# Kernel optimization log

Measured on AMD Instinct MI355X. Metric: run time of the kernel, lower is better.

Reference implementation:

```python
import jax, jax.numpy as jnp
import numpy as np
from jax import lax

B, N, T, H, V, C = 256, 196, 26, 512, 12000, 1000


def setup_inputs() -> dict:
    key = jax.random.key(0)
    ks = jax.random.split(key, 24)
    g = lambda i, shape, s=0.02: jax.random.normal(ks[i], shape, jnp.float32) * s
    z = lambda *shape: jnp.zeros(shape, jnp.float32)
    return {
        "image": jax.random.normal(ks[0], (B, N, H), jnp.float32),
        "question": jax.random.randint(ks[1], (B, T), 0, V, jnp.int32),
        "embed_table": g(2, (V, H), 1.0),
        "W_img": g(3, (H, H)), "b_img": z(H),
        "W_uni": g(4, (1, H, H)), "b_uni": z(H),
        "W_bi": g(5, (2, H, H)), "b_bi": z(H),
        "W_tri": g(6, (3, H, H)), "b_tri": z(H),
        "lstm_k": g(7, (H, 4 * H)), "lstm_rk": g(8, (H, 4 * H)), "lstm_b": z(4 * H),
        "W_corr": g(9, (H, H)), "b_corr": z(H),
        "W_qe": g(10, (H, H)), "b_qe": z(H),
        "W_ie": g(11, (H, H)), "b_ie": z(H),
        "w_qa": g(12, (H, 1)), "b_qa": z(1),
        "w_ia": g(13, (H, 1)), "b_ia": z(1),
        "W_w": g(14, (H, H)), "b_w": z(H),
        "W_p": g(15, (2 * H, H)), "b_p": z(H),
        "W_s": g(16, (2 * H, H)), "b_s": z(H),
        "W_fc1": g(17, (H, 2 * H)), "b_fc1": z(2 * H),
        "W_fc": g(18, (2 * H, C)), "b_fc": z(C),
    }


def _conv1d(x, w, b, dil):
    # x: [B,T,H], w: [k, in, out] (WIO). TF 'same' padding == XLA SAME.
    y = lax.conv_general_dilated(x, w, window_strides=(1,), padding='SAME',
                                 rhs_dilation=(dil,),
                                 dimension_numbers=('NWC', 'WIO', 'NWC'))
    return y + b


def _lstm(x, k, rk, b):
    # Keras LSTM, gate order i,f,c,o; inference (dropout off).
    xp = jnp.einsum('bth,hg->btg', x, k) + b  # [B,T,4H]
    h0 = jnp.zeros((x.shape[0], rk.shape[0]), x.dtype)

    def step(carry, xt):
        h, c = carry
        zg = xt + h @ rk
        i, f, g, o = jnp.split(zg, 4, axis=-1)
        i, f, o = jax.nn.sigmoid(i), jax.nn.sigmoid(f), jax.nn.sigmoid(o)
        c = f * c + i * jnp.tanh(g)
        h = o * jnp.tanh(c)
        return (h, c), h

    _, hs = lax.scan(step, (h0, h0), jnp.swapaxes(xp, 0, 1))
    return jnp.swapaxes(hs, 0, 1)  # [B,T,H]


def _co_attention(img_feat, ques_feat, W_corr, b_corr, W_qe, b_qe, W_ie, b_ie,
                  w_qa, b_qa, w_ia, b_ia):
    img_corr = img_feat @ W_corr + b_corr                       # [B,N,H]
    wm = jnp.tanh(jnp.einsum('btd,bnd->btn', ques_feat, img_corr))  # affinity
    ques_embed = ques_feat @ W_qe + b_qe                        # [B,T,H]
    img_embed = img_feat @ W_ie + b_ie                          # [B,N,H]
    ques_sum = jnp.tanh(jnp.einsum('btn,bnd->btd', wm, img_embed) + ques_embed)
    ques_att = jax.nn.softmax((ques_sum @ w_qa + b_qa)[..., 0], axis=-1)  # [B,T]
    img_sum = jnp.tanh(jnp.einsum('btn,btd->bnd', wm, ques_embed) + img_embed)
    img_att = jax.nn.softmax((img_sum @ w_ia + b_ia)[..., 0], axis=-1)    # [B,N]
    q_feat = jnp.einsum('bt,btd->bd', ques_att, ques_feat)
    v_feat = jnp.einsum('bn,bnd->bd', img_att, img_feat)
    return v_feat, q_feat


def reference(image, question, embed_table, W_img, b_img, W_uni, b_uni, W_bi, b_bi,
              W_tri, b_tri, lstm_k, lstm_rk, lstm_b, W_corr, b_corr, W_qe, b_qe,
              W_ie, b_ie, w_qa, b_qa, w_ia, b_ia, W_w, b_w, W_p, b_p, W_s, b_s,
              W_fc1, b_fc1, W_fc, b_fc):
    img = jnp.tanh(image @ W_img + b_img)                       # [B,N,H]
    words = embed_table[question]                               # [B,T,H]
    uni = jnp.tanh(_conv1d(words, W_uni, b_uni, 1))
    bi = jnp.tanh(_conv1d(words, W_bi, b_bi, 2))
    tri = jnp.tanh(_conv1d(words, W_tri, b_tri, 2))
    phrase = jnp.tanh(jnp.maximum(jnp.maximum(uni, bi), tri))   # maxpool over 3 n-grams
    sentence = _lstm(phrase, lstm_k, lstm_rk, lstm_b)
    ca = lambda v, q: _co_attention(v, q, W_corr, b_corr, W_qe, b_qe, W_ie, b_ie,
                                    w_qa, b_qa, w_ia, b_ia)
    v_word, q_word = ca(img, words)
    v_phr, q_phr = ca(img, phrase)
    v_sent, q_sent = ca(img, sentence)
    h_w = jnp.tanh((q_word + v_word) @ W_w + b_w)
    h_p = jnp.tanh(jnp.concatenate([q_phr + v_phr, h_w], axis=1) @ W_p + b_p)
    h_s = jnp.tanh(jnp.concatenate([q_sent + v_sent, h_p], axis=1) @ W_s + b_s)
    fc1 = jax.nn.relu(h_s @ W_fc1 + b_fc1)
    return jax.nn.softmax(fc1 @ W_fc + b_fc, axis=-1)           # [B,C]
```

## Files before the change

### kernel.cpp

```cpp
#include <hip/hip_runtime.h>
#include <hip/hip_bf16.h>
#include <math.h>

#define Bq   256
#define Nimg 196
#define Tseq 26
#define Hd   512
#define H4   2048
#define Ccls 1000
#define KP   1536

typedef int   int4v  __attribute__((ext_vector_type(4)));
typedef float f32x4  __attribute__((ext_vector_type(4)));

#define SWZ8(x) ((x) ^ (((x) >> 3) & 7))

__device__ __forceinline__ float fast_tanh(float x) {
    float e = __expf(2.0f * x);
    return 1.0f - 2.0f * __builtin_amdgcn_rcpf(e + 1.0f);
}
__device__ __forceinline__ float fast_sigmoid(float x) {
    return __builtin_amdgcn_rcpf(1.0f + __expf(-x));
}

__device__ __forceinline__ short f2bf(float x) {
    union { float f; unsigned u; } a; a.f = x;
    unsigned r = a.u + 0x7FFF + ((a.u >> 16) & 1);
    return (short)(r >> 16);
}
__device__ __forceinline__ float bf2f(short b) {
    union { float f; unsigned u; } a; a.u = ((unsigned)(unsigned short)b) << 16;
    return a.f;
}

__global__ void embed_kernel(const int* __restrict__ q, const float* __restrict__ table,
                             short* __restrict__ words2) {
    int row = blockIdx.x;
    int tok = q[row];
    int c4 = threadIdx.x * 4;
    float4 v = *reinterpret_cast<const float4*>(table + (size_t)tok * Hd + c4);
    short h0 = f2bf(v.x), h1 = f2bf(v.y), h2 = f2bf(v.z), h3 = f2bf(v.w);
    short l0 = f2bf(v.x - bf2f(h0)), l1 = f2bf(v.y - bf2f(h1));
    short l2 = f2bf(v.z - bf2f(h2)), l3 = f2bf(v.w - bf2f(h3));
    *reinterpret_cast<short4*>(words2 + (size_t)row * 1024 + c4) = make_short4(h0, h1, h2, h3);
    *reinterpret_cast<short4*>(words2 + (size_t)row * 1024 + 512 + c4) = make_short4(l0, l1, l2, l3);
}

__global__ void split_kernel(const float* __restrict__ X, short* __restrict__ X2) {
    int i4 = blockIdx.x * 256 + threadIdx.x;
    int m = i4 >> 7, c4 = (i4 & 127) * 4;
    float4 v = *reinterpret_cast<const float4*>(X + ((size_t)m << 9) + c4);
    short h0 = f2bf(v.x), h1 = f2bf(v.y), h2 = f2bf(v.z), h3 = f2bf(v.w);
    short l0 = f2bf(v.x - bf2f(h0)), l1 = f2bf(v.y - bf2f(h1));
    short l2 = f2bf(v.z - bf2f(h2)), l3 = f2bf(v.w - bf2f(h3));
    *reinterpret_cast<short4*>(X2 + (size_t)m * 1024 + c4) = make_short4(h0, h1, h2, h3);
    *reinterpret_cast<short4*>(X2 + (size_t)m * 1024 + 512 + c4) = make_short4(l0, l1, l2, l3);
}

__global__ __launch_bounds__(256) void wsplit_kernel(const float* __restrict__ W, int Nw,
                                                     short* __restrict__ WT2) {
    __shared__ float tile[64][65];
    const int n0 = blockIdx.x * 64, k0 = blockIdx.y * 64;
    const int tid = threadIdx.x;
    #pragma unroll
    for (int p = 0; p < 16; ++p) {
        int r = p * 4 + (tid >> 6);
        int c = tid & 63;
        tile[r][c] = W[(size_t)(k0 + r) * Nw + n0 + c];
    }
    __syncthreads();
    const int n = tid >> 2;
    const int ksub = (tid & 3) * 16;
    size_t base = (size_t)(n0 + n) * KP + k0 + ksub;
    #pragma unroll
    for (int k = 0; k < 16; ++k) {
        float x = tile[ksub + k][n];
        short h = f2bf(x);
        short l = f2bf(x - bf2f(h));
        WT2[base + k] = h;
        WT2[base + 512 + k] = h;
        WT2[base + 1024 + k] = l;
    }
}

__device__ __forceinline__ void mfma16(f32x4& acc, int4v a, int4v b) {
    asm volatile("v_mfma_f32_16x16x32_bf16 %0, %1, %2, %0" : "+v"(acc) : "v"(a), "v"(b));
}

template <int ACT, int OUT, int SWZ>
__global__ __launch_bounds__(256) void mfma_gemm_kernel(
    const short* __restrict__ A2, const short* __restrict__ W2T,
    const float* __restrict__ bias, float* __restrict__ C, short* __restrict__ C2,
    int M, int N) {
    __shared__ __align__(16) short Asl[2][4096];
    __shared__ __align__(16) short Bsl[2][4096];
    const int tid = threadIdx.x;
    const int lane = tid & 63, wid = tid >> 6;
    int row0, col0;
    if (SWZ) {
        const int P8 = (M >> 7) >> 3;
        const int Cn = N >> 7;
        int L = blockIdx.x;
        int xcd = L & 7, slot = L >> 3;
        row0 = (xcd * P8 + slot / Cn) << 7;
        col0 = (slot % Cn) << 7;
    } else {
        row0 = blockIdx.y * 128;
        col0 = blockIdx.x * 128;
    }
    const int wm = wid >> 1, wn = wid & 1;
    const short* ab[2]; const short* bb[2]; int koff[2];
    #pragma unroll
    for (int c = 0; c < 2; ++c) {
        int d = c * 256 + tid;
        int s = SWZ8(d);
        int fr = s >> 6, r = (s >> 2) & 15, kb = s & 3;
        koff[c] = kb * 8;
        ab[c] = A2 + (size_t)(row0 + fr * 16 + r) * 1024;
        bb[c] = W2T + (size_t)(col0 + fr * 16 + r) * KP;
    }
    auto STAGE = [&](int buf, int k0) {
        #pragma unroll
        for (int c = 0; c < 2; ++c) {
            int kk = k0 + koff[c];
            int ka = kk >= 1024 ? kk - 1024 : kk;
            __builtin_amdgcn_global_load_lds(
                (const __attribute__((address_space(1))) void*)(ab[c] + ka),
                (__attribute__((address_space(3))) void*)(&Asl[buf][(c * 256 + wid * 64) * 8]),
                16, 0, 0);
            __builtin_amdgcn_global_load_lds(
                (const __attribute__((address_space(1))) void*)(bb[c] + kk),
                (__attribute__((address_space(3))) void*)(&Bsl[buf][(c * 256 + wid * 64) * 8]),
                16, 0, 0);
        }
    };
    f32x4 acc[4][4] = {};
    STAGE(0, 0);
    int cur = 0;
    for (int k0 = 0; k0 < KP; k0 += 32) {
        if (k0 + 32 < KP) {
            STAGE(cur ^ 1, k0 + 32);
            asm volatile("s_waitcnt vmcnt(4)" ::: "memory");
        } else {
            asm volatile("s_waitcnt vmcnt(0)" ::: "memory");
        }
        __builtin_amdgcn_s_barrier();
        __builtin_amdgcn_sched_barrier(0);
        int4v af[4], bfr[4];
        #pragma unroll
        for (int f = 0; f < 4; ++f) {
            int sa = (wm * 4 + f) * 64 + (lane & 15) * 4 + (lane >> 4);
            af[f] = *reinterpret_cast<const int4v*>(&Asl[cur][SWZ8(sa) * 8]);
            int sb = (wn * 4 + f) * 64 + (lane & 15) * 4 + (lane >> 4);
            bfr[f] = *reinterpret_cast<const int4v*>(&Bsl[cur][SWZ8(sb) * 8]);
        }
        #pragma unroll
        for (int i = 0; i < 4; ++i)
            #pragma unroll
            for (int j = 0; j < 4; ++j)
                mfma16(acc[i][j], af[i], bfr[j]);
        asm volatile("s_waitcnt lgkmcnt(0)" ::: "memory");
        __builtin_amdgcn_s_barrier();
        __builtin_amdgcn_sched_barrier(0);
        cur ^= 1;
    }
    asm volatile("s_nop 7\n\ts_nop 7" ::: "memory");
    #pragma unroll
    for (int i = 0; i < 4; ++i) {
        #pragma unroll
        for (int j = 0; j < 4; ++j) {
            int colj = col0 + wn * 64 + j * 16 + (lane & 15);
            float bv = bias ? bias[colj] : 0.f;
            #pragma unroll
            for (int r = 0; r < 4; ++r) {
                int row = row0 + wm * 64 + i * 16 + (lane >> 4) * 4 + r;
                float v = acc[i][j][r] + bv;
                if (ACT == 1) v = fast_tanh(v);
                if (OUT == 0) {
                    C[(size_t)row * N + colj] = v;
                } else {
                    short h = f2bf(v), l = f2bf(v - bf2f(h));
                    C2[(size_t)row * 1024 + colj] = h;
                    C2[(size_t)row * 1024 + 512 + colj] = l;
                }
            }
        }
    }
}

__global__ __launch_bounds__(256) void wm3_mfma_kernel(
    const short* __restrict__ Q0, const short* __restrict__ Q1, const short* __restrict__ Q2,
    const short* __restrict__ icS2, float* __restrict__ wm0, float* __restrict__ wm1,
    float* __restrict__ wm2) {
    __shared__ __align__(16) short Asl[2][4096];
    __shared__ __align__(16) short Bsl[2][4096];
    const int tid = threadIdx.x;
    const int lane = tid & 63, wid = tid >> 6;
    const int col0 = blockIdx.x * 128;
    const int b = blockIdx.y;
    const int wmq = wid >> 1, wn = wid & 1;
    const short* Qsrc[3] = {Q0, Q1, Q2};
    const short* ab[2]; const short* bb[2]; int koff[2];
    #pragma unroll
    for (int c = 0; c < 2; ++c) {
        int d = c * 256 + tid;
        int s = SWZ8(d);
        int fr = s >> 6, r = (s >> 2) & 15, kb = s & 3;
        koff[c] = kb * 8;
        int arow = fr * 16 + r;
        int lvl = arow / 26, at = arow - lvl * 26;
        if (arow >= 78) { lvl = 0; at = 0; }
        ab[c] = Qsrc[lvl] + ((size_t)(b * 26 + at)) * 1024;
        int brow = col0 + fr * 16 + r;
        if (brow > 195) brow = 195;
        bb[c] = icS2 + ((size_t)(b * 196 + brow)) * 1024;
    }
    auto STAGE = [&](int buf, int k0) {
        #pragma unroll
        for (int c = 0; c < 2; ++c) {
            int kk = k0 + koff[c];
            int ka = kk >= 1024 ? kk - 1024 : kk;
            int kbv = kk >= 512 ? kk - 512 : kk;
            __builtin_amdgcn_global_load_lds(
                (const __attribute__((address_space(1))) void*)(ab[c] + ka),
                (__attribute__((address_space(3))) void*)(&Asl[buf][(c * 256 + wid * 64) * 8]),
                16, 0, 0);
            __builtin_amdgcn_global_load_lds(
                (const __attribute__((address_space(1))) void*)(bb[c] + kbv),
                (__attribute__((address_space(3))) void*)(&Bsl[buf][(c * 256 + wid * 64) * 8]),
                16, 0, 0);
        }
    };
    f32x4 acc[4][4] = {};
    STAGE(0, 0);
    int cur = 0;
    for (int k0 = 0; k0 < KP; k0 += 32) {
        if (k0 + 32 < KP) {
            STAGE(cur ^ 1, k0 + 32);
            asm volatile("s_waitcnt vmcnt(4)" ::: "memory");
        } else {
            asm volatile("s_waitcnt vmcnt(0)" ::: "memory");
        }
        __builtin_amdgcn_s_barrier();
        __builtin_amdgcn_sched_barrier(0);
        int4v af[4], bfr[4];
        #pragma unroll
        for (int f = 0; f < 4; ++f) {
            int sa = (wmq * 4 + f) * 64 + (lane & 15) * 4 + (lane >> 4);
            af[f] = *reinterpret_cast<const int4v*>(&Asl[cur][SWZ8(sa) * 8]);
            int sb = (wn * 4 + f) * 64 + (lane & 15) * 4 + (lane >> 4);
            bfr[f] = *reinterpret_cast<const int4v*>(&Bsl[cur][SWZ8(sb) * 8]);
        }
        #pragma unroll
        for (int i = 0; i < 4; ++i)
            #pragma unroll
            for (int j = 0; j < 4; ++j)
                mfma16(acc[i][j], af[i], bfr[j]);
        asm volatile("s_waitcnt lgkmcnt(0)" ::: "memory");
        __builtin_amdgcn_s_barrier();
        __builtin_amdgcn_sched_barrier(0);
        cur ^= 1;
    }
    asm volatile("s_nop 7\n\ts_nop 7" ::: "memory");
    #pragma unroll
    for (int i = 0; i < 4; ++i) {
        #pragma unroll
        for (int j = 0; j < 4; ++j) {
            int col = col0 + wn * 64 + j * 16 + (lane & 15);
            if (col >= Nimg) continue;
            #pragma unroll
            for (int r = 0; r < 4; ++r) {
                int row = wmq * 64 + i * 16 + (lane >> 4) * 4 + r;
                if (row >= 78) continue;
                int lvl = row / 26, t = row - lvl * 26;
                float* dst = (lvl == 0) ? wm0 : (lvl == 1) ? wm1 : wm2;
                dst[((size_t)(b * 26 + t)) * Nimg + col] = fast_tanh(acc[i][j][r]);
            }
        }
    }
}

__global__ void conv_combine_kernel(const float* __restrict__ Y,
                                    const float* __restrict__ bu, const float* __restrict__ bb,
                                    const float* __restrict__ bt,
                                    short* __restrict__ phrase2) {
    int idx = blockIdx.x * 256 + threadIdx.x;
    int m = idx >> 9, c = idx & 511;
    int t = m % Tseq;
    const float* Ym = Y + (size_t)m * 3072;
    float u = Ym[c] + bu[c];
    float bv = bb[c];
    if (t > 0)  bv += Ym[-3072 + 512 + c];
    if (t < 25) bv += Ym[3072 + 1024 + c];
    float tv = Ym[2048 + c] + bt[c];
    if (t > 1)  tv += Ym[-6144 + 1536 + c];
    if (t < 24) tv += Ym[6144 + 2560 + c];
    float ph = fast_tanh(fmaxf(fmaxf(fast_tanh(u), fast_tanh(bv)), fast_tanh(tv)));
    short h = f2bf(ph), l = f2bf(ph - bf2f(h));
    phrase2[(size_t)m * 1024 + c] = h;
    phrase2[(size_t)m * 1024 + 512 + c] = l;
}

template <int ACT>
__global__ __launch_bounds__(256) void gemm_kernel(
    const float* __restrict__ A, int lda,
    const float* __restrict__ W, int ldw,
    const float* __restrict__ bias,
    float* __restrict__ C, int ldc,
    int M, int Ncols, int K) {
    __shared__ float As[16][68];
    __shared__ float Ws[16][68];
    const int tid = threadIdx.x;
    const int tx4 = (tid & 15) * 4, ty4 = (tid >> 4) * 4;
    const int row0 = blockIdx.y * 64, col0 = blockIdx.x * 64;
    const int am = tid >> 2, ak = (tid & 3) * 4;
    const int wk = tid >> 4, wc = (tid & 15) * 4;
    float acc[4][4] = {};
    for (int k0 = 0; k0 < K; k0 += 16) {
        {
            int gr = row0 + am;
            float4 v = make_float4(0.f, 0.f, 0.f, 0.f);
            if (gr < M) v = *reinterpret_cast<const float4*>(A + (size_t)gr * lda + k0 + ak);
            As[ak + 0][am] = v.x; As[ak + 1][am] = v.y; As[ak + 2][am] = v.z; As[ak + 3][am] = v.w;
        }
        {
            int gc = col0 + wc;
            const float* wp = W + (size_t)(k0 + wk) * ldw + gc;
            float4 v = make_float4(0.f, 0.f, 0.f, 0.f);
            if (gc + 3 < Ncols) v = *reinterpret_cast<const float4*>(wp);
            else {
                if (gc + 0 < Ncols) v.x = wp[0];
                if (gc + 1 < Ncols) v.y = wp[1];
                if (gc + 2 < Ncols) v.z = wp[2];
                if (gc + 3 < Ncols) v.w = wp[3];
            }
            Ws[wk][wc + 0] = v.x; Ws[wk][wc + 1] = v.y; Ws[wk][wc + 2] = v.z; Ws[wk][wc + 3] = v.w;
        }
        __syncthreads();
        #pragma unroll 4
        for (int kk = 0; kk < 16; ++kk) {
            float4 a4 = *reinterpret_cast<const float4*>(&As[kk][ty4]);
            float4 b4 = *reinterpret_cast<const float4*>(&Ws[kk][tx4]);
            float a[4] = {a4.x, a4.y, a4.z, a4.w};
            float b[4] = {b4.x, b4.y, b4.z, b4.w};
            #pragma unroll
            for (int i = 0; i < 4; ++i)
                #pragma unroll
                for (int j = 0; j < 4; ++j) acc[i][j] += a[i] * b[j];
        }
        __syncthreads();
    }
    #pragma unroll
    for (int i = 0; i < 4; ++i) {
        int r = row0 + ty4 + i;
        if (r >= M) continue;
        #pragma unroll
        for (int j = 0; j < 4; ++j) {
            int c = col0 + tx4 + j;
            if (c >= Ncols) continue;
            float v = acc[i][j];
            if (bias) v += bias[c];
            if (ACT == 1) v = fast_tanh(v);
            else if (ACT == 2) v = fmaxf(v, 0.f);
            C[(size_t)r * ldc + c] = v;
        }
    }
}

__global__ __launch_bounds__(256) void lstm_gemm_kernel(
    const float* __restrict__ h, const float* __restrict__ rk, float* __restrict__ zgp) {
    __shared__ float As[16][68];
    __shared__ float Ws[16][68];
    const int tid = threadIdx.x;
    const int tx4 = (tid & 15) * 4, ty4 = (tid >> 4) * 4;
    const int col0 = blockIdx.x * 64, row0 = blockIdx.y * 64, kb = blockIdx.z * 256;
    const int am = tid >> 2, ak = (tid & 3) * 4;
    const int wk = tid >> 4, wc = (tid & 15) * 4;
    float acc[4][4] = {};
    for (int k0 = kb; k0 < kb + 256; k0 += 16) {
        {
            float4 v = *reinterpret_cast<const float4*>(h + (size_t)(row0 + am) * Hd + k0 + ak);
            As[ak + 0][am] = v.x; As[ak + 1][am] = v.y; As[ak + 2][am] = v.z; As[ak + 3][am] = v.w;
        }
        {
            *reinterpret_cast<float4*>(&Ws[wk][wc]) =
                *reinterpret_cast<const float4*>(rk + (size_t)(k0 + wk) * H4 + col0 + wc);
        }
        __syncthreads();
        #pragma unroll 4
        for (int kk = 0; kk < 16; ++kk) {
            float4 a4 = *reinterpret_cast<const float4*>(&As[kk][ty4]);
            float4 b4 = *reinterpret_cast<const float4*>(&Ws[kk][tx4]);
            float a[4] = {a4.x, a4.y, a4.z, a4.w};
            float b[4] = {b4.x, b4.y, b4.z, b4.w};
            #pragma unroll
            for (int i = 0; i < 4; ++i)
                #pragma unroll
                for (int j = 0; j < 4; ++j) acc[i][j] += a[i] * b[j];
        }
        __syncthreads();
    }
    float* dst = zgp + (size_t)blockIdx.z * (Bq * H4);
    #pragma unroll
    for (int i = 0; i < 4; ++i) {
        int r = row0 + ty4 + i;
        *reinterpret_cast<float4*>(dst + (size_t)r * H4 + col0 + tx4) =
            make_float4(acc[i][0], acc[i][1], acc[i][2], acc[i][3]);
    }
}

__global__ __launch_bounds__(256) void lstm_gates_kernel(
    const float* __restrict__ zgp, const float* __restrict__ xp,
    float* __restrict__ c, float* __restrict__ h, short* __restrict__ sent2, int t) {
    int i = blockIdx.x * 256 + threadIdx.x;
    int b = i >> 9, hh = i & 511;
    const float* xr = xp + ((size_t)b * Tseq + t) * H4;
    float z[4];
    #pragma unroll
    for (int g = 0; g < 4; ++g) {
        float s = xr[g * 512 + hh];
        #pragma unroll
        for (int kc = 0; kc < 2; ++kc)
            s += zgp[(size_t)kc * (Bq * H4) + (size_t)b * H4 + g * 512 + hh];
        z[g] = s;
    }
    float ig = fast_sigmoid(z[0]);
    float fg = fast_sigmoid(z[1]);
    float gg = fast_tanh(z[2]);
    float og = fast_sigmoid(z[3]);
    float cv = fg * c[i] + ig * gg;
    c[i] = cv;
    float hv = og * fast_tanh(cv);
    h[i] = hv;
    short hb = f2bf(hv), lb = f2bf(hv - bf2f(hb));
    sent2[((size_t)b * Tseq + t) * 1024 + hh] = hb;
    sent2[((size_t)b * Tseq + t) * 1024 + 512 + hh] = lb;
}

__global__ __launch_bounds__(256) void qlog3_kernel(
    const float* __restrict__ wm0, const float* __restrict__ wm1, const float* __restrict__ wm2,
    const float* __restrict__ Ie, const float* __restrict__ qe0, const float* __restrict__ qe1,
    const float* __restrict__ qe2, const float* __restrict__ wqa, float* __restrict__ qlogp) {
    const int b = blockIdx.x, chunk = blockIdx.y;
    __shared__ float wms[3][Tseq][Nimg];
    __shared__ float red[4][40];
    const int tid = threadIdx.x;
    const float* wsrc[3] = {wm0, wm1, wm2};
    for (int e = tid; e < 3 * 1274; e += 256) {
        int c = e / 1274, r = e % 1274;
        *reinterpret_cast<float4*>(&wms[c][0][0] + 4 * r) =
            *reinterpret_cast<const float4*>(wsrc[c] + (size_t)b * (Tseq * Nimg) + 4 * r);
    }
    __syncthreads();
    const int hl = tid & 127, thalf = tid >> 7, tt0 = thalf * 13;
    const int h1 = chunk * 256 + hl, h2 = h1 + 128;
    float acc[3][13][2] = {};
    const float* iep1 = Ie + (size_t)b * Nimg * Hd + h1;
    const float* iep2 = Ie + (size_t)b * Nimg * Hd + h2;
    for (int n4 = 0; n4 < 49; ++n4) {
        float ieA0 = iep1[(size_t)(4 * n4 + 0) * Hd];
        float ieA1 = iep1[(size_t)(4 * n4 + 1) * Hd];
        float ieA2 = iep1[(size_t)(4 * n4 + 2) * Hd];
        float ieA3 = iep1[(size_t)(4 * n4 + 3) * Hd];
        float ieB0 = iep2[(size_t)(4 * n4 + 0) * Hd];
        float ieB1 = iep2[(size_t)(4 * n4 + 1) * Hd];
        float ieB2 = iep2[(size_t)(4 * n4 + 2) * Hd];
        float ieB3 = iep2[(size_t)(4 * n4 + 3) * Hd];
        #pragma unroll
        for (int c = 0; c < 3; ++c)
            #pragma unroll
            for (int tt = 0; tt < 13; ++tt) {
                float4 w4 = *reinterpret_cast<const float4*>(&wms[c][tt0 + tt][4 * n4]);
                acc[c][tt][0] += w4.x * ieA0 + w4.y * ieA1 + w4.z * ieA2 + w4.w * ieA3;
                acc[c][tt][1] += w4.x * ieB0 + w4.y * ieB1 + w4.z * ieB2 + w4.w * ieB3;
            }
    }
    const float wq1 = wqa[h1], wq2 = wqa[h2];
    const int lane = tid & 63, w = tid >> 6;
    const float* qes[3] = {qe0, qe1, qe2};
    #pragma unroll
    for (int c = 0; c < 3; ++c)
        #pragma unroll
        for (int tt = 0; tt < 13; ++tt) {
            int t = tt0 + tt;
            const float* qrow = qes[c] + ((size_t)(b * 26 + t)) * Hd;
            float v = fast_tanh(acc[c][tt][0] + qrow[h1]) * wq1 +
                      fast_tanh(acc[c][tt][1] + qrow[h2]) * wq2;
            #pragma unroll
            for (int off = 32; off; off >>= 1) v += __shfl_xor(v, off);
            if (lane == 0) red[w][c * 13 + tt] = v;
        }
    __syncthreads();
    if (tid < 39) {
        int c = tid / 13, tt = tid % 13;
        qlogp[((size_t)c * Bq + b) * (2 * 26) + chunk * 26 + tt] = red[0][tid] + red[1][tid];
    } else if (tid >= 64 && tid < 103) {
        int id = tid - 64;
        int c = id / 13, tt = id % 13;
        qlogp[((size_t)c * Bq + b) * (2 * 26) + chunk * 26 + 13 + tt] = red[2][id] + red[3][id];
    }
}

__global__ __launch_bounds__(256) void ilog_kernel(
    const float* __restrict__ wm, const float* __restrict__ qe,
    const float* __restrict__ Ie, const float* __restrict__ wia,
    float* __restrict__ ilog) {
    const int b = blockIdx.x, nbase = blockIdx.y * 98;
    __shared__ float qes[Tseq][516];
    __shared__ float wms[Tseq][100];
    const int tid = threadIdx.x;
    for (int e = tid; e < Tseq * 128; e += 256) {
        int t = e >> 7, q4 = (e & 127) * 4;
        *reinterpret_cast<float4*>(&qes[t][q4]) =
            *reinterpret_cast<const float4*>(qe + ((size_t)(b * 26 + t)) * Hd + q4);
    }
    for (int e = tid; e < Tseq * 98; e += 256) {
        int t = e / 98, n = e % 98;
        wms[t][n] = wm[((size_t)(b * 26 + t)) * Nimg + nbase + n];
    }
    __syncthreads();
    const int lane = tid & 63, w = tid >> 6;
    float4 wi0 = *reinterpret_cast<const float4*>(wia + 4 * lane);
    float4 wi1 = *reinterpret_cast<const float4*>(wia + 256 + 4 * lane);
    for (int n = w; n < 98; n += 4) {
        float4 a0 = make_float4(0.f, 0.f, 0.f, 0.f);
        float4 a1 = make_float4(0.f, 0.f, 0.f, 0.f);
        #pragma unroll 13
        for (int t = 0; t < Tseq; ++t) {
            float wmv = wms[t][n];
            float4 q0 = *reinterpret_cast<const float4*>(&qes[t][4 * lane]);
            float4 q1 = *reinterpret_cast<const float4*>(&qes[t][256 + 4 * lane]);
            a0.x += wmv * q0.x; a0.y += wmv * q0.y; a0.z += wmv * q0.z; a0.w += wmv * q0.w;
            a1.x += wmv * q1.x; a1.y += wmv * q1.y; a1.z += wmv * q1.z; a1.w += wmv * q1.w;
        }
        const float* iebn = Ie + ((size_t)(b * Nimg) + nbase + n) * Hd;
        float4 e0 = *reinterpret_cast<const float4*>(iebn + 4 * lane);
        float4 e1 = *reinterpret_cast<const float4*>(iebn + 256 + 4 * lane);
        float v = fast_tanh(a0.x + e0.x) * wi0.x + fast_tanh(a0.y + e0.y) * wi0.y +
                  fast_tanh(a0.z + e0.z) * wi0.z + fast_tanh(a0.w + e0.w) * wi0.w +
                  fast_tanh(a1.x + e1.x) * wi1.x + fast_tanh(a1.y + e1.y) * wi1.y +
                  fast_tanh(a1.z + e1.z) * wi1.z + fast_tanh(a1.w + e1.w) * wi1.w;
        #pragma unroll
        for (int off = 32; off; off >>= 1) v += __shfl_xor(v, off);
        if (lane == 0) ilog[(size_t)b * Nimg + nbase + n] = v;
    }
}

__global__ void softmaxT_part_kernel(const float* __restrict__ lgp, float* __restrict__ att) {
    int b = blockIdx.x, lane = threadIdx.x;
    float v = -INFINITY;
    if (lane < Tseq) {
        const float* p = lgp + (size_t)b * (2 * 26) + lane;
        v = p[0] + p[26];
    }
    float m = v;
    #pragma unroll
    for (int off = 32; off; off >>= 1) m = fmaxf(m, __shfl_xor(m, off));
    float e = (lane < Tseq) ? __expf(v - m) : 0.f;
    float s = e;
    #pragma unroll
    for (int off = 32; off; off >>= 1) s += __shfl_xor(s, off);
    if (lane < Tseq) att[(size_t)b * Tseq + lane] = e / s;
}

__global__ void softmax_N_kernel(const float* __restrict__ lg, float* __restrict__ att) {
    int b = blockIdx.x, lane = threadIdx.x;
    float v[4]; float m = -INFINITY;
    #pragma unroll
    for (int k = 0; k < 4; ++k) {
        int n = lane + 64 * k;
        v[k] = (n < Nimg) ? lg[(size_t)b * Nimg + n] : -INFINITY;
        m = fmaxf(m, v[k]);
    }
    #pragma unroll
    for (int off = 32; off; off >>= 1) m = fmaxf(m, __shfl_xor(m, off));
    float e[4]; float s = 0.f;
    #pragma unroll
    for (int k = 0; k < 4; ++k) {
        int n = lane + 64 * k;
        e[k] = (n < Nimg) ? __expf(v[k] - m) : 0.f;
        s += e[k];
    }
    #pragma unroll
    for (int off = 32; off; off >>= 1) s += __shfl_xor(s, off);
    #pragma unroll
    for (int k = 0; k < 4; ++k) {
        int n = lane + 64 * k;
        if (n < Nimg) att[(size_t)b * Nimg + n] = e[k] / s;
    }
}

__global__ __launch_bounds__(256) void feat3_kernel(
    const float* __restrict__ qatt0, const float* __restrict__ qatt1, const float* __restrict__ qatt2,
    const float* __restrict__ iatt0, const float* __restrict__ iatt1, const float* __restrict__ iatt2,
    const short* __restrict__ Qw2, const short* __restrict__ Qp2, const short* __restrict__ Qs2,
    const short* __restrict__ img2, float* __restrict__ s_part) {
    const int b = blockIdx.x, chunk = blockIdx.y, tid = threadIdx.x;
    float a[3][2] = {};
    if (chunk == 0) {
        for (int t = 0; t < Tseq; ++t) {
            float w0 = qatt0[b * Tseq + t], w1 = qatt1[b * Tseq + t], w2 = qatt2[b * Tseq + t];
            const short* p0 = Qw2 + ((size_t)(b * Tseq + t)) * 1024;
            const short* p1 = Qp2 + ((size_t)(b * Tseq + t)) * 1024;
            const short* p2 = Qs2 + ((size_t)(b * Tseq + t)) * 1024;
            a[0][0] += w0 * (bf2f(p0[tid]) + bf2f(p0[512 + tid]));
            a[0][1] += w0 * (bf2f(p0[256 + tid]) + bf2f(p0[768 + tid]));
            a[1][0] += w1 * (bf2f(p1[tid]) + bf2f(p1[512 + tid]));
            a[1][1] += w1 * (bf2f(p1[256 + tid]) + bf2f(p1[768 + tid]));
            a[2][0] += w2 * (bf2f(p2[tid]) + bf2f(p2[512 + tid]));
            a[2][1] += w2 * (bf2f(p2[256 + tid]) + bf2f(p2[768 + tid]));
        }
    }
    int ns, ne;
    if (chunk == 0)      { ns = 0;   ne = 30;  }
    else if (chunk == 1) { ns = 30;  ne = 86;  }
    else if (chunk == 2) { ns = 86;  ne = 141; }
    else                 { ns = 141; ne = 196; }
    for (int n = ns; n < ne; ++n) {
        float w0 = iatt0[b * Nimg + n], w1 = iatt1[b * Nimg + n], w2 = iatt2[b * Nimg + n];
        const short* p = img2 + ((size_t)(b * Nimg) + n) * 1024;
        float v0 = bf2f(p[tid]) + bf2f(p[512 + tid]);
        float v1 = bf2f(p[256 + tid]) + bf2f(p[768 + tid]);
        a[0][0] += w0 * v0; a[0][1] += w0 * v1;
        a[1][0] += w1 * v0; a[1][1] += w1 * v1;
        a[2][0] += w2 * v0; a[2][1] += w2 * v1;
    }
    #pragma unroll
    for (int c = 0; c < 3; ++c) {
        float* dst = s_part + ((size_t)(chunk * 3 + c) * Bq + b) * Hd;
        dst[tid] = a[c][0];
        dst[tid + 256] = a[c][1];
    }
}

__global__ void feat_combine_kernel(const float* __restrict__ s_part, float* __restrict__ s0,
                                    float* __restrict__ s1, float* __restrict__ s2) {
    int i = blockIdx.x * 256 + threadIdx.x;
    int c = i / (Bq * Hd), r = i % (Bq * Hd);
    float v = 0.f;
    #pragma unroll
    for (int ch = 0; ch < 4; ++ch) v += s_part[(size_t)(ch * 3 + c) * (Bq * Hd) + r];
    float* dst = (c == 0) ? s0 : (c == 1) ? s1 : s2;
    dst[r] = v;
}

__global__ void concat_kernel(const float* __restrict__ x, const float* __restrict__ y,
                              float* __restrict__ out) {
    int i = blockIdx.x * 256 + threadIdx.x;
    int b = i >> 9, j = i & 511;
    out[(size_t)b * 1024 + j] = x[i];
    out[(size_t)b * 1024 + 512 + j] = y[i];
}

__global__ __launch_bounds__(256) void softmax_C_kernel(const float* __restrict__ lg,
                                                        float* __restrict__ out) {
    int b = blockIdx.x, tid = threadIdx.x;
    __shared__ float red[4];
    const float* lb = lg + (size_t)b * Ccls;
    float v[4]; float m = -INFINITY;
    #pragma unroll
    for (int k = 0; k < 4; ++k) {
        int j = tid + 256 * k;
        v[k] = (j < Ccls) ? lb[j] : -INFINITY;
        m = fmaxf(m, v[k]);
    }
    #pragma unroll
    for (int off = 32; off; off >>= 1) m = fmaxf(m, __shfl_xor(m, off));
    int lane = tid & 63, w = tid >> 6;
    if (lane == 0) red[w] = m;
    __syncthreads();
    m = fmaxf(fmaxf(red[0], red[1]), fmaxf(red[2], red[3]));
    __syncthreads();
    float e[4]; float s = 0.f;
    #pragma unroll
    for (int k = 0; k < 4; ++k) {
        int j = tid + 256 * k;
        e[k] = (j < Ccls) ? __expf(v[k] - m) : 0.f;
        s += e[k];
    }
    #pragma unroll
    for (int off = 32; off; off >>= 1) s += __shfl_xor(s, off);
    if (lane == 0) red[w] = s;
    __syncthreads();
    s = red[0] + red[1] + red[2] + red[3];
    float inv = 1.f / s;
    #pragma unroll
    for (int k = 0; k < 4; ++k) {
        int j = tid + 256 * k;
        if (j < Ccls) out[(size_t)b * Ccls + j] = e[k] * inv;
    }
}

extern "C" void kernel_launch(void* const* d_in, const int* in_sizes, int n_in,
                              void* d_out, int out_size, void* d_ws, size_t ws_size,
                              hipStream_t stream) {
    const float* image   = (const float*)d_in[0];
    const int*   question= (const int*)  d_in[1];
    const float* embed   = (const float*)d_in[2];
    const float* W_img   = (const float*)d_in[3];
    const float* b_img   = (const float*)d_in[4];
    const float* W_uni   = (const float*)d_in[5];
    const float* b_uni   = (const float*)d_in[6];
    const float* W_bi    = (const float*)d_in[7];
    const float* b_bi    = (const float*)d_in[8];
    const float* W_tri   = (const float*)d_in[9];
    const float* b_tri   = (const float*)d_in[10];
    const float* lstm_k  = (const float*)d_in[11];
    const float* lstm_rk = (const float*)d_in[12];
    const float* lstm_b  = (const float*)d_in[13];
    const float* W_corr  = (const float*)d_in[14];
    const float* b_corr  = (const float*)d_in[15];
    const float* W_qe    = (const float*)d_in[16];
    const float* b_qe    = (const float*)d_in[17];
    const float* W_ie    = (const float*)d_in[18];
    const float* b_ie    = (const float*)d_in[19];
    const float* w_qa    = (const float*)d_in[20];
    const float* w_ia    = (const float*)d_in[22];
    const float* W_w     = (const float*)d_in[24];
    const float* b_w     = (const float*)d_in[25];
    const float* W_p     = (const float*)d_in[26];
    const float* b_p     = (const float*)d_in[27];
    const float* W_s     = (const float*)d_in[28];
    const float* b_s     = (const float*)d_in[29];
    const float* W_fc1   = (const float*)d_in[30];
    const float* b_fc1   = (const float*)d_in[31];
    const float* W_fc    = (const float*)d_in[32];
    const float* b_fc    = (const float*)d_in[33];

    float* p = (float*)d_ws;
    size_t off = 0;
    auto take = [&](size_t n) { float* r = p + off; off += n; return r; };
    auto take_s = [&](size_t n) { short* r = (short*)(p + off); off += n / 2; return r; };
    float* bufB   = take((size_t)Bq * Nimg * Hd);
    float* xp     = take((size_t)Bq * Tseq * H4);
    float* wm0    = take((size_t)Bq * Tseq * Nimg);
    float* wm1    = take((size_t)Bq * Tseq * Nimg);
    float* wm2    = take((size_t)Bq * Tseq * Nimg);
    float* hbuf   = take((size_t)Bq * Hd);
    float* cbuf   = take((size_t)Bq * Hd);
    float* zgp    = take((size_t)2 * Bq * H4);
    float* qlogp  = take((size_t)3 * Bq * 4 * Tseq);
    float* qatt0  = take((size_t)Bq * Tseq);
    float* qatt1  = take((size_t)Bq * Tseq);
    float* qatt2  = take((size_t)Bq * Tseq);
    float* ilogb  = take((size_t)Bq * Nimg);
    float* iatt0  = take((size_t)Bq * Nimg);
    float* iatt1  = take((size_t)Bq * Nimg);
    float* iatt2  = take((size_t)Bq * Nimg);
    short* imgS2   = take_s((size_t)Bq * Nimg * 1024);
    short* words2  = take_s((size_t)Bq * Tseq * 1024);
    short* phrase2 = take_s((size_t)Bq * Tseq * 1024);
    short* sentn2  = take_s((size_t)Bq * Tseq * 1024);
    short* WimgT2  = take_s((size_t)Hd * KP);
    short* WcorrT2 = take_s((size_t)Hd * KP);
    short* WieT2   = take_s((size_t)Hd * KP);
    short* WqeT2   = take_s((size_t)Hd * KP);
    short* WconvT2 = take_s((size_t)6 * Hd * KP);
    short* lkT2    = take_s((size_t)H4 * KP);

    float* qe0 = xp;
    float* qe1 = xp + (size_t)Bq * Tseq * Hd;
    float* qe2 = xp + 2 * (size_t)Bq * Tseq * Hd;
    float* s_part = xp + 3 * (size_t)Bq * Tseq * Hd;
    float* Y      = bufB;
    short* image2 = (short*)bufB;
    short* icS2   = (short*)bufB;
    float* catb   = wm0;
    float* fc1b   = wm0 + (size_t)Bq * 2 * Hd;
    float* logits = wm0 + 2 * (size_t)Bq * 2 * Hd;
    float* s0     = wm1;
    float* s1     = wm1 + 1 * (size_t)Bq * Hd;
    float* s2     = wm1 + 2 * (size_t)Bq * Hd;
    float* hw     = wm1 + 3 * (size_t)Bq * Hd;
    float* hp     = wm1 + 4 * (size_t)Bq * Hd;
    float* hsv    = wm1 + 5 * (size_t)Bq * Hd;

    const int MI = Bq * Nimg;
    const int MT = Bq * Tseq;

    wsplit_kernel<<<dim3(8, 8), 256, 0, stream>>>(W_img, Hd, WimgT2);
    wsplit_kernel<<<dim3(8, 8), 256, 0, stream>>>(W_corr, Hd, WcorrT2);
    wsplit_kernel<<<dim3(8, 8), 256, 0, stream>>>(W_ie, Hd, WieT2);
    wsplit_kernel<<<dim3(8, 8), 256, 0, stream>>>(W_qe, Hd, WqeT2);
    wsplit_kernel<<<dim3(8, 8), 256, 0, stream>>>(W_uni, Hd, WconvT2 + 0 * (size_t)Hd * KP);
    wsplit_kernel<<<dim3(8, 8), 256, 0, stream>>>(W_bi, Hd, WconvT2 + 1 * (size_t)Hd * KP);
    wsplit_kernel<<<dim3(8, 8), 256, 0, stream>>>(W_bi + (size_t)Hd * Hd, Hd, WconvT2 + 2 * (size_t)Hd * KP);
    wsplit_kernel<<<dim3(8, 8), 256, 0, stream>>>(W_tri, Hd, WconvT2 + 3 * (size_t)Hd * KP);
    wsplit_kernel<<<dim3(8, 8), 256, 0, stream>>>(W_tri + (size_t)Hd * Hd, Hd, WconvT2 + 4 * (size_t)Hd * KP);
    wsplit_kernel<<<dim3(8, 8), 256, 0, stream>>>(W_tri + 2 * (size_t)Hd * Hd, Hd, WconvT2 + 5 * (size_t)Hd * KP);
    wsplit_kernel<<<dim3(32, 8), 256, 0, stream>>>(lstm_k, H4, lkT2);

    embed_kernel<<<MT, 128, 0, stream>>>(question, embed, words2);
    split_kernel<<<MI / 2, 256, 0, stream>>>(image, image2);
    mfma_gemm_kernel<1, 1, 1><<<dim3((MI / 128) * (Hd / 128)), 256, 0, stream>>>(
        image2, WimgT2, b_img, nullptr, imgS2, MI, Hd);
    mfma_gemm_kernel<0, 0, 0><<<dim3(3072 / 128, MT / 128), 256, 0, stream>>>(
        words2, WconvT2, nullptr, Y, nullptr, MT, 3072);
    conv_combine_kernel<<<(MT * Hd) / 256, 256, 0, stream>>>(Y, b_uni, b_bi, b_tri, phrase2);
    mfma_gemm_kernel<0, 0, 0><<<dim3(H4 / 128, MT / 128), 256, 0, stream>>>(
        phrase2, lkT2, lstm_b, xp, nullptr, MT, H4);
    hipMemsetAsync(hbuf, 0, (size_t)Bq * Hd * sizeof(float), stream);
    hipMemsetAsync(cbuf, 0, (size_t)Bq * Hd * sizeof(float), stream);
    for (int t = 0; t < Tseq; ++t) {
        lstm_gemm_kernel<<<dim3(32, 4, 2), 256, 0, stream>>>(hbuf, lstm_rk, zgp);
        lstm_gates_kernel<<<(Bq * Hd) / 256, 256, 0, stream>>>(zgp, xp, cbuf, hbuf, sentn2, t);
    }
    mfma_gemm_kernel<0, 1, 1><<<dim3((MI / 128) * (Hd / 128)), 256, 0, stream>>>(
        imgS2, WcorrT2, b_corr, nullptr, icS2, MI, Hd);
    wm3_mfma_kernel<<<dim3(2, Bq), 256, 0, stream>>>(words2, phrase2, sentn2, icS2,
                                                     wm0, wm1, wm2);
    mfma_gemm_kernel<0, 0, 1><<<dim3((MI / 128) * (Hd / 128)), 256, 0, stream>>>(
        imgS2, WieT2, b_ie, bufB, nullptr, MI, Hd);
    mfma_gemm_kernel<0, 0, 0><<<dim3(Hd / 128, (3 * MT) / 128), 256, 0, stream>>>(
        words2, WqeT2, b_qe, qe0, nullptr, 3 * MT, Hd);
    qlog3_kernel<<<dim3(Bq, 2), 256, 0, stream>>>(wm0, wm1, wm2, bufB, qe0, qe1, qe2, w_qa, qlogp);
    softmaxT_part_kernel<<<Bq, 64, 0, stream>>>(qlogp + 0 * (size_t)Bq * 2 * Tseq, qatt0);
    softmaxT_part_kernel<<<Bq, 64, 0, stream>>>(qlogp + 1 * (size_t)Bq * 2 * Tseq, qatt1);
    softmaxT_part_kernel<<<Bq, 64, 0, stream>>>(qlogp + 2 * (size_t)Bq * 2 * Tseq, qatt2);
    ilog_kernel<<<dim3(Bq, 2), 256, 0, stream>>>(wm0, qe0, bufB, w_ia, ilogb);
    softmax_N_kernel<<<Bq, 64, 0, stream>>>(ilogb, iatt0);
    ilog_kernel<<<dim3(Bq, 2), 256, 0, stream>>>(wm1, qe1, bufB, w_ia, ilogb);
    softmax_N_kernel<<<Bq, 64, 0, stream>>>(ilogb, iatt1);
    ilog_kernel<<<dim3(Bq, 2), 256, 0, stream>>>(wm2, qe2, bufB, w_ia, ilogb);
    softmax_N_kernel<<<Bq, 64, 0, stream>>>(ilogb, iatt2);
    feat3_kernel<<<dim3(Bq, 4), 256, 0, stream>>>(qatt0, qatt1, qatt2, iatt0, iatt1, iatt2,
                                                  words2, phrase2, sentn2, imgS2, s_part);
    feat_combine_kernel<<<(3 * Bq * Hd) / 256, 256, 0, stream>>>(s_part, s0, s1, s2);
    gemm_kernel<1><<<dim3(Hd / 64, Bq / 64), 256, 0, stream>>>(
        s0, Hd, W_w, Hd, b_w, hw, Hd, Bq, Hd, Hd);
    concat_kernel<<<(Bq * Hd) / 256, 256, 0, stream>>>(s1, hw, catb);
    gemm_kernel<1><<<dim3(Hd / 64, Bq / 64), 256, 0, stream>>>(
        catb, 2 * Hd, W_p, Hd, b_p, hp, Hd, Bq, Hd, 2 * Hd);
    concat_kernel<<<(Bq * Hd) / 256, 256, 0, stream>>>(s2, hp, catb);
    gemm_kernel<1><<<dim3(Hd / 64, Bq / 64), 256, 0, stream>>>(
        catb, 2 * Hd, W_s, Hd, b_s, hsv, Hd, Bq, Hd, 2 * Hd);
    gemm_kernel<2><<<dim3((2 * Hd) / 64, Bq / 64), 256, 0, stream>>>(
        hsv, Hd, W_fc1, 2 * Hd, b_fc1, fc1b, 2 * Hd, Bq, 2 * Hd, Hd);
    gemm_kernel<0><<<dim3((Ccls + 63) / 64, Bq / 64), 256, 0, stream>>>(
        fc1b, 2 * Hd, W_fc, Ccls, b_fc, logits, Ccls, Bq, Ccls, 2 * Hd);
    softmax_C_kernel<<<Bq, 256, 0, stream>>>(logits, (float*)d_out);
}
```

Measured before the change: 1.947 ms.

## Double MFMA GEMM K-tile to 64 and batch small per-level kernels

```diff
diff --git a/kernel.cpp b/kernel.cpp
--- a/kernel.cpp
+++ b/kernel.cpp
@@ -57,10 +57,37 @@
     *reinterpret_cast<short4*>(X2 + (size_t)m * 1024 + 512 + c4) = make_short4(l0, l1, l2, l3);
 }
 
-__global__ __launch_bounds__(256) void wsplit_kernel(const float* __restrict__ W, int Nw,
-                                                     short* __restrict__ WT2) {
+__global__ __launch_bounds__(256) void wsplit_all_kernel(
+    const float* __restrict__ W_img, const float* __restrict__ W_corr,
+    const float* __restrict__ W_ie, const float* __restrict__ W_qe,
+    const float* __restrict__ W_uni, const float* __restrict__ W_bi,
+    const float* __restrict__ W_tri, const float* __restrict__ lstm_k,
+    short* __restrict__ WimgT2, short* __restrict__ WcorrT2,
+    short* __restrict__ WieT2, short* __restrict__ WqeT2,
+    short* __restrict__ WconvT2, short* __restrict__ lkT2) {
+    const int z = blockIdx.z;
+    const float* W; short* WT2; int Nw, n0;
+    const size_t HK = (size_t)Hd * KP;
+    if (z < 10) {
+        Nw = Hd; n0 = blockIdx.x * 64;
+        switch (z) {
+            case 0: W = W_img;  WT2 = WimgT2;  break;
+            case 1: W = W_corr; WT2 = WcorrT2; break;
+            case 2: W = W_ie;   WT2 = WieT2;   break;
+            case 3: W = W_qe;   WT2 = WqeT2;   break;
+            case 4: W = W_uni;                     WT2 = WconvT2 + 0 * HK; break;
+            case 5: W = W_bi;                      WT2 = WconvT2 + 1 * HK; break;
+            case 6: W = W_bi + (size_t)Hd * Hd;    WT2 = WconvT2 + 2 * HK; break;
+            case 7: W = W_tri;                     WT2 = WconvT2 + 3 * HK; break;
+            case 8: W = W_tri + (size_t)Hd * Hd;   WT2 = WconvT2 + 4 * HK; break;
+            default:W = W_tri + 2 * (size_t)Hd * Hd; WT2 = WconvT2 + 5 * HK; break;
+        }
+    } else {
+        Nw = H4; W = lstm_k; WT2 = lkT2;
+        n0 = ((z - 10) * 8 + blockIdx.x) * 64;
+    }
     __shared__ float tile[64][65];
-    const int n0 = blockIdx.x * 64, k0 = blockIdx.y * 64;
+    const int k0 = blockIdx.y * 64;
     const int tid = threadIdx.x;
     #pragma unroll
     for (int p = 0; p < 16; ++p) {
@@ -92,8 +119,8 @@
     const short* __restrict__ A2, const short* __restrict__ W2T,
     const float* __restrict__ bias, float* __restrict__ C, short* __restrict__ C2,
     int M, int N) {
-    __shared__ __align__(16) short Asl[2][4096];
-    __shared__ __align__(16) short Bsl[2][4096];
+    __shared__ __align__(16) short Asl[2][8192];
+    __shared__ __align__(16) short Bsl[2][8192];
     const int tid = threadIdx.x;
     const int lane = tid & 63, wid = tid >> 6;
     int row0, col0;
@@ -109,56 +136,59 @@
         col0 = blockIdx.x * 128;
     }
     const int wm = wid >> 1, wn = wid & 1;
-    const short* ab[2]; const short* bb[2]; int koff[2];
-    #pragma unroll
-    for (int c = 0; c < 2; ++c) {
+    const short* ab[4]; const short* bb[4]; int koff[4];
+    #pragma unroll
+    for (int c = 0; c < 4; ++c) {
         int d = c * 256 + tid;
         int s = SWZ8(d);
-        int fr = s >> 6, r = (s >> 2) & 15, kb = s & 3;
+        int fr = s >> 7, r = (s >> 3) & 15, kb = s & 7;
         koff[c] = kb * 8;
         ab[c] = A2 + (size_t)(row0 + fr * 16 + r) * 1024;
         bb[c] = W2T + (size_t)(col0 + fr * 16 + r) * KP;
     }
     auto STAGE = [&](int buf, int k0) {
         #pragma unroll
-        for (int c = 0; c < 2; ++c) {
+        for (int c = 0; c < 4; ++c) {
             int kk = k0 + koff[c];
             int ka = kk >= 1024 ? kk - 1024 : kk;
             __builtin_amdgcn_global_load_lds(
                 (const __attribute__((address_space(1))) void*)(ab[c] + ka),
-                (__attribute__((address_space(3))) void*)(&Asl[buf][(c * 256 + wid * 64) * 8]),
+                (__attribute__((address_space(3))) void*)(&Asl[buf][(c * 256 + tid) * 8]),
                 16, 0, 0);
             __builtin_amdgcn_global_load_lds(
                 (const __attribute__((address_space(1))) void*)(bb[c] + kk),
-                (__attribute__((address_space(3))) void*)(&Bsl[buf][(c * 256 + wid * 64) * 8]),
+                (__attribute__((address_space(3))) void*)(&Bsl[buf][(c * 256 + tid) * 8]),
                 16, 0, 0);
         }
     };
     f32x4 acc[4][4] = {};
     STAGE(0, 0);
     int cur = 0;
-    for (int k0 = 0; k0 < KP; k0 += 32) {
-        if (k0 + 32 < KP) {
-            STAGE(cur ^ 1, k0 + 32);
-            asm volatile("s_waitcnt vmcnt(4)" ::: "memory");
+    for (int k0 = 0; k0 < KP; k0 += 64) {
+        if (k0 + 64 < KP) {
+            STAGE(cur ^ 1, k0 + 64);
+            asm volatile("s_waitcnt vmcnt(8)" ::: "memory");
         } else {
             asm volatile("s_waitcnt vmcnt(0)" ::: "memory");
         }
         __builtin_amdgcn_s_barrier();
         __builtin_amdgcn_sched_barrier(0);
-        int4v af[4], bfr[4];
-        #pragma unroll
-        for (int f = 0; f < 4; ++f) {
-            int sa = (wm * 4 + f) * 64 + (lane & 15) * 4 + (lane >> 4);
-            af[f] = *reinterpret_cast<const int4v*>(&Asl[cur][SWZ8(sa) * 8]);
-            int sb = (wn * 4 + f) * 64 + (lane & 15) * 4 + (lane >> 4);
-            bfr[f] = *reinterpret_cast<const int4v*>(&Bsl[cur][SWZ8(sb) * 8]);
-        }
-        #pragma unroll
-        for (int i = 0; i < 4; ++i)
-            #pragma unroll
-            for (int j = 0; j < 4; ++j)
-                mfma16(acc[i][j], af[i], bfr[j]);
+        #pragma unroll
+        for (int ks = 0; ks < 2; ++ks) {
+            int4v af[4], bfr[4];
+            #pragma unroll
+            for (int f = 0; f < 4; ++f) {
+                int sa = (wm * 4 + f) * 128 + (lane & 15) * 8 + ks * 4 + (lane >> 4);
+                af[f] = *reinterpret_cast<const int4v*>(&Asl[cur][SWZ8(sa) * 8]);
+                int sb = (wn * 4 + f) * 128 + (lane & 15) * 8 + ks * 4 + (lane >> 4);
+                bfr[f] = *reinterpret_cast<const int4v*>(&Bsl[cur][SWZ8(sb) * 8]);
+            }
+            #pragma unroll
+            for (int i = 0; i < 4; ++i)
+                #pragma unroll
+                for (int j = 0; j < 4; ++j)
+                    mfma16(acc[i][j], af[i], bfr[j]);
+        }
         asm volatile("s_waitcnt lgkmcnt(0)" ::: "memory");
         __builtin_amdgcn_s_barrier();
         __builtin_amdgcn_sched_barrier(0);
@@ -192,20 +222,20 @@
     const short* __restrict__ Q0, const short* __restrict__ Q1, const short* __restrict__ Q2,
     const short* __restrict__ icS2, float* __restrict__ wm0, float* __restrict__ wm1,
     float* __restrict__ wm2) {
-    __shared__ __align__(16) short Asl[2][4096];
-    __shared__ __align__(16) short Bsl[2][4096];
+    __shared__ __align__(16) short Asl[2][8192];
+    __shared__ __align__(16) short Bsl[2][8192];
     const int tid = threadIdx.x;
     const int lane = tid & 63, wid = tid >> 6;
     const int col0 = blockIdx.x * 128;
     const int b = blockIdx.y;
     const int wmq = wid >> 1, wn = wid & 1;
     const short* Qsrc[3] = {Q0, Q1, Q2};
-    const short* ab[2]; const short* bb[2]; int koff[2];
-    #pragma unroll
-    for (int c = 0; c < 2; ++c) {
+    const short* ab[4]; const short* bb[4]; int koff[4];
+    #pragma unroll
+    for (int c = 0; c < 4; ++c) {
         int d = c * 256 + tid;
         int s = SWZ8(d);
-        int fr = s >> 6, r = (s >> 2) & 15, kb = s & 3;
+        int fr = s >> 7, r = (s >> 3) & 15, kb = s & 7;
         koff[c] = kb * 8;
         int arow = fr * 16 + r;
         int lvl = arow / 26, at = arow - lvl * 26;
@@ -217,45 +247,48 @@
     }
     auto STAGE = [&](int buf, int k0) {
         #pragma unroll
-        for (int c = 0; c < 2; ++c) {
+        for (int c = 0; c < 4; ++c) {
             int kk = k0 + koff[c];
             int ka = kk >= 1024 ? kk - 1024 : kk;
             int kbv = kk >= 512 ? kk - 512 : kk;
             __builtin_amdgcn_global_load_lds(
                 (const __attribute__((address_space(1))) void*)(ab[c] + ka),
-                (__attribute__((address_space(3))) void*)(&Asl[buf][(c * 256 + wid * 64) * 8]),
+                (__attribute__((address_space(3))) void*)(&Asl[buf][(c * 256 + tid) * 8]),
                 16, 0, 0);
             __builtin_amdgcn_global_load_lds(
                 (const __attribute__((address_space(1))) void*)(bb[c] + kbv),
-                (__attribute__((address_space(3))) void*)(&Bsl[buf][(c * 256 + wid * 64) * 8]),
+                (__attribute__((address_space(3))) void*)(&Bsl[buf][(c * 256 + tid) * 8]),
                 16, 0, 0);
         }
     };
     f32x4 acc[4][4] = {};
     STAGE(0, 0);
     int cur = 0;
-    for (int k0 = 0; k0 < KP; k0 += 32) {
-        if (k0 + 32 < KP) {
-            STAGE(cur ^ 1, k0 + 32);
-            asm volatile("s_waitcnt vmcnt(4)" ::: "memory");
+    for (int k0 = 0; k0 < KP; k0 += 64) {
+        if (k0 + 64 < KP) {
+            STAGE(cur ^ 1, k0 + 64);
+            asm volatile("s_waitcnt vmcnt(8)" ::: "memory");
         } else {
             asm volatile("s_waitcnt vmcnt(0)" ::: "memory");
         }
         __builtin_amdgcn_s_barrier();
         __builtin_amdgcn_sched_barrier(0);
-        int4v af[4], bfr[4];
-        #pragma unroll
-        for (int f = 0; f < 4; ++f) {
-            int sa = (wmq * 4 + f) * 64 + (lane & 15) * 4 + (lane >> 4);
-            af[f] = *reinterpret_cast<const int4v*>(&Asl[cur][SWZ8(sa) * 8]);
-            int sb = (wn * 4 + f) * 64 + (lane & 15) * 4 + (lane >> 4);
-            bfr[f] = *reinterpret_cast<const int4v*>(&Bsl[cur][SWZ8(sb) * 8]);
-        }
-        #pragma unroll
-        for (int i = 0; i < 4; ++i)
-            #pragma unroll
-            for (int j = 0; j < 4; ++j)
-                mfma16(acc[i][j], af[i], bfr[j]);
+        #pragma unroll
+        for (int ks = 0; ks < 2; ++ks) {
+            int4v af[4], bfr[4];
+            #pragma unroll
+            for (int f = 0; f < 4; ++f) {
+                int sa = (wmq * 4 + f) * 128 + (lane & 15) * 8 + ks * 4 + (lane >> 4);
+                af[f] = *reinterpret_cast<const int4v*>(&Asl[cur][SWZ8(sa) * 8]);
+                int sb = (wn * 4 + f) * 128 + (lane & 15) * 8 + ks * 4 + (lane >> 4);
+                bfr[f] = *reinterpret_cast<const int4v*>(&Bsl[cur][SWZ8(sb) * 8]);
+            }
+            #pragma unroll
+            for (int i = 0; i < 4; ++i)
+                #pragma unroll
+                for (int j = 0; j < 4; ++j)
+                    mfma16(acc[i][j], af[i], bfr[j]);
+        }
         asm volatile("s_waitcnt lgkmcnt(0)" ::: "memory");
         __builtin_amdgcn_s_barrier();
         __builtin_amdgcn_sched_barrier(0);
@@ -501,11 +534,14 @@
     }
 }
 
-__global__ __launch_bounds__(256) void ilog_kernel(
-    const float* __restrict__ wm, const float* __restrict__ qe,
+__global__ __launch_bounds__(256) void ilog3_kernel(
+    const float* __restrict__ wmb, const float* __restrict__ qeb,
     const float* __restrict__ Ie, const float* __restrict__ wia,
-    float* __restrict__ ilog) {
-    const int b = blockIdx.x, nbase = blockIdx.y * 98;
+    float* __restrict__ ilog3) {
+    const int b = blockIdx.x, nbase = blockIdx.y * 98, lvl = blockIdx.z;
+    const float* wm = wmb + (size_t)lvl * Bq * Tseq * Nimg;
+    const float* qe = qeb + (size_t)lvl * Bq * Tseq * Hd;
+    float* ilog = ilog3 + (size_t)lvl * Bq * Nimg;
     __shared__ float qes[Tseq][516];
     __shared__ float wms[Tseq][100];
     const int tid = threadIdx.x;
@@ -547,10 +583,10 @@
 }
 
 __global__ void softmaxT_part_kernel(const float* __restrict__ lgp, float* __restrict__ att) {
-    int b = blockIdx.x, lane = threadIdx.x;
+    int b = blockIdx.x, c = blockIdx.y, lane = threadIdx.x;
     float v = -INFINITY;
     if (lane < Tseq) {
-        const float* p = lgp + (size_t)b * (2 * 26) + lane;
+        const float* p = lgp + ((size_t)c * Bq + b) * (2 * 26) + lane;
         v = p[0] + p[26];
     }
     float m = v;
@@ -560,16 +596,18 @@
     float s = e;
     #pragma unroll
     for (int off = 32; off; off >>= 1) s += __shfl_xor(s, off);
-    if (lane < Tseq) att[(size_t)b * Tseq + lane] = e / s;
+    if (lane < Tseq) att[((size_t)c * Bq + b) * Tseq + lane] = e / s;
 }
 
 __global__ void softmax_N_kernel(const float* __restrict__ lg, float* __restrict__ att) {
-    int b = blockIdx.x, lane = threadIdx.x;
+    int b = blockIdx.x, c = blockIdx.y, lane = threadIdx.x;
+    const float* lb = lg + ((size_t)c * Bq + b) * Nimg;
+    float* ab = att + ((size_t)c * Bq + b) * Nimg;
     float v[4]; float m = -INFINITY;
     #pragma unroll
     for (int k = 0; k < 4; ++k) {
         int n = lane + 64 * k;
-        v[k] = (n < Nimg) ? lg[(size_t)b * Nimg + n] : -INFINITY;
+        v[k] = (n < Nimg) ? lb[n] : -INFINITY;
         m = fmaxf(m, v[k]);
     }
     #pragma unroll
@@ -586,7 +624,7 @@
     #pragma unroll
     for (int k = 0; k < 4; ++k) {
         int n = lane + 64 * k;
-        if (n < Nimg) att[(size_t)b * Nimg + n] = e[k] / s;
+        if (n < Nimg) ab[n] = e[k] / s;
     }
 }
 
@@ -743,7 +781,7 @@
     float* qatt0  = take((size_t)Bq * Tseq);
     float* qatt1  = take((size_t)Bq * Tseq);
     float* qatt2  = take((size_t)Bq * Tseq);
-    float* ilogb  = take((size_t)Bq * Nimg);
+    float* ilog3  = take((size_t)3 * Bq * Nimg);
     float* iatt0  = take((size_t)Bq * Nimg);
     float* iatt1  = take((size_t)Bq * Nimg);
     float* iatt2  = take((size_t)Bq * Nimg);
@@ -778,17 +816,9 @@
     const int MI = Bq * Nimg;
     const int MT = Bq * Tseq;
 
-    wsplit_kernel<<<dim3(8, 8), 256, 0, stream>>>(W_img, Hd, WimgT2);
-    wsplit_kernel<<<dim3(8, 8), 256, 0, stream>>>(W_corr, Hd, WcorrT2);
-    wsplit_kernel<<<dim3(8, 8), 256, 0, stream>>>(W_ie, Hd, WieT2);
-    wsplit_kernel<<<dim3(8, 8), 256, 0, stream>>>(W_qe, Hd, WqeT2);
-    wsplit_kernel<<<dim3(8, 8), 256, 0, stream>>>(W_uni, Hd, WconvT2 + 0 * (size_t)Hd * KP);
-    wsplit_kernel<<<dim3(8, 8), 256, 0, stream>>>(W_bi, Hd, WconvT2 + 1 * (size_t)Hd * KP);
-    wsplit_kernel<<<dim3(8, 8), 256, 0, stream>>>(W_bi + (size_t)Hd * Hd, Hd, WconvT2 + 2 * (size_t)Hd * KP);
-    wsplit_kernel<<<dim3(8, 8), 256, 0, stream>>>(W_tri, Hd, WconvT2 + 3 * (size_t)Hd * KP);
-    wsplit_kernel<<<dim3(8, 8), 256, 0, stream>>>(W_tri + (size_t)Hd * Hd, Hd, WconvT2 + 4 * (size_t)Hd * KP);
-    wsplit_kernel<<<dim3(8, 8), 256, 0, stream>>>(W_tri + 2 * (size_t)Hd * Hd, Hd, WconvT2 + 5 * (size_t)Hd * KP);
-    wsplit_kernel<<<dim3(32, 8), 256, 0, stream>>>(lstm_k, H4, lkT2);
+    wsplit_all_kernel<<<dim3(8, 8, 14), 256, 0, stream>>>(
+        W_img, W_corr, W_ie, W_qe, W_uni, W_bi, W_tri, lstm_k,
+        WimgT2, WcorrT2, WieT2, WqeT2, WconvT2, lkT2);
 
     embed_kernel<<<MT, 128, 0, stream>>>(question, embed, words2);
     split_kernel<<<MI / 2, 256, 0, stream>>>(image, image2);
@@ -814,15 +844,9 @@
     mfma_gemm_kernel<0, 0, 0><<<dim3(Hd / 128, (3 * MT) / 128), 256, 0, stream>>>(
         words2, WqeT2, b_qe, qe0, nullptr, 3 * MT, Hd);
     qlog3_kernel<<<dim3(Bq, 2), 256, 0, stream>>>(wm0, wm1, wm2, bufB, qe0, qe1, qe2, w_qa, qlogp);
-    softmaxT_part_kernel<<<Bq, 64, 0, stream>>>(qlogp + 0 * (size_t)Bq * 2 * Tseq, qatt0);
-    softmaxT_part_kernel<<<Bq, 64, 0, stream>>>(qlogp + 1 * (size_t)Bq * 2 * Tseq, qatt1);
-    softmaxT_part_kernel<<<Bq, 64, 0, stream>>>(qlogp + 2 * (size_t)Bq * 2 * Tseq, qatt2);
-    ilog_kernel<<<dim3(Bq, 2), 256, 0, stream>>>(wm0, qe0, bufB, w_ia, ilogb);
-    softmax_N_kernel<<<Bq, 64, 0, stream>>>(ilogb, iatt0);
-    ilog_kernel<<<dim3(Bq, 2), 256, 0, stream>>>(wm1, qe1, bufB, w_ia, ilogb);
-    softmax_N_kernel<<<Bq, 64, 0, stream>>>(ilogb, iatt1);
-    ilog_kernel<<<dim3(Bq, 2), 256, 0, stream>>>(wm2, qe2, bufB, w_ia, ilogb);
-    softmax_N_kernel<<<Bq, 64, 0, stream>>>(ilogb, iatt2);
+    softmaxT_part_kernel<<<dim3(Bq, 3), 64, 0, stream>>>(qlogp, qatt0);
+    ilog3_kernel<<<dim3(Bq, 2, 3), 256, 0, stream>>>(wm0, qe0, bufB, w_ia, ilog3);
+    softmax_N_kernel<<<dim3(Bq, 3), 64, 0, stream>>>(ilog3, iatt0);
     feat3_kernel<<<dim3(Bq, 4), 256, 0, stream>>>(qatt0, qatt1, qatt2, iatt0, iatt1, iatt2,
                                                   words2, phrase2, sentn2, imgS2, s_part);
     feat_combine_kernel<<<(3 * Bq * Hd) / 256, 256, 0, stream>>>(s_part, s0, s1, s2);
```

New measurement: 1.987 ms. +2.0%, slower.
